# Optimization experiments

Measured on AMD Instinct MI355X. Metric: run time of the kernel, lower is better.

Reference implementation:

```python
import jax, jax.numpy as jnp
import numpy as np

K = 3        # num patches
S = 2        # scale factor
G = 32       # base glimpse size


def _avg_pool(x, k):
    # x: (b, c, H, W), kernel=stride=k (matches F.avg_pool2d(x, k))
    if k == 1:
        return x
    b, c, h, w = x.shape
    return x.reshape(b, c, h // k, k, w // k, k).mean(axis=(3, 5))


def _extract_patch(x, l, size):
    # x: (b, c, h, w); l: (b, 2) in [-1, 1]; returns (b, c, size, size)
    b, c, h, w = x.shape
    start = (0.5 * ((l + 1.0) * h)).astype(jnp.int32)  # (b, 2) [col, row]
    pad = size // 2 + 1
    xp = jnp.pad(x, ((0, 0), (0, 0), (pad, pad), (pad, pad)))

    def slice_one(img, st):
        # img: (c, hp, wp); st: (2,) -> rows use st[1], cols use st[0]
        return jax.lax.dynamic_slice(img, (0, st[1], st[0]), (c, size, size))

    return jax.vmap(slice_one)(xp, start)


def _foveate(x, l):
    phi = []
    size = G
    for _ in range(K):
        phi.append(_extract_patch(x, l, size))
        size = int(S * size)
    # pool every coarser patch back to GxG, concat on channel, flatten
    phi = [_avg_pool(p, p.shape[-1] // G) for p in phi]
    phi = jnp.concatenate(phi, axis=1)          # (b, K*c, G, G)
    return phi.reshape(phi.shape[0], -1)        # (b, K*c*G*G)


def setup_inputs() -> dict:
    key = jax.random.key(0)
    ks = jax.random.split(key, 10)
    b, c, h, w = 256, 3, 224, 224
    h_g = h_l = 1024
    dim = K * G * G * c  # 9216
    x = jax.random.normal(ks[0], (b, c, h, w), dtype=jnp.float32)
    l_prev = jax.random.uniform(ks[1], (b, 2), dtype=jnp.float32, minval=-1.0, maxval=1.0)
    def lin(k, fan_in, fan_out):
        return jax.random.normal(k, (fan_in, fan_out), dtype=jnp.float32) / np.sqrt(fan_in)
    return {
        "x": x, "l_prev": l_prev,
        "W1": lin(ks[2], dim, h_g), "b1": jnp.zeros((h_g,), jnp.float32),
        "W2": lin(ks[3], 2, h_l),   "b2": jnp.zeros((h_l,), jnp.float32),
        "W3": lin(ks[4], h_g, h_g + h_l), "b3": jnp.zeros((h_g + h_l,), jnp.float32),
        "W4": lin(ks[5], h_l, h_g + h_l), "b4": jnp.zeros((h_g + h_l,), jnp.float32),
    }


def reference(x, l_prev, W1, b1, W2, b2, W3, b3, W4, b4):
    glimpse = _foveate(x, l_prev)                       # (b, K*c*G*G)
    g_out = jax.nn.relu(glimpse @ W1 + b1)              # (b, h_g)
    l_out = jax.nn.relu(l_prev @ W2 + b2)               # (b, h_l)
    what = g_out @ W3 + b3                              # (b, h_g+h_l)
    where = l_out @ W4 + b4                             # (b, h_g+h_l)
    return jax.nn.relu(what + where)
```

## Files before the change

### kernel.cpp

```cpp
#include <hip/hip_runtime.h>

typedef __bf16 bf16_t;
typedef __bf16 bf16x8 __attribute__((ext_vector_type(8)));
typedef float f32x4 __attribute__((ext_vector_type(4)));
typedef unsigned short us4 __attribute__((ext_vector_type(4)));
typedef unsigned short us8 __attribute__((ext_vector_type(8)));

template<int F>
__device__ __forceinline__ void fov_scale(const float* __restrict__ xb,
                                          bf16_t* __restrict__ gb,
                                          int r0, int c0, int base, int count, int kidx)
{
  constexpr float inv = 1.0f / (F * F);
  for (int i = threadIdx.x; i < count; i += 256) {
    const int idx = base + i;
    const int ch  = idx >> 10;
    const int rem = idx & 1023;
    const int gy  = rem >> 5, gx = rem & 31;
    const float* xc = xb + ch * 50176;
    float sum = 0.0f;
    const int rbase = r0 + gy * F, cbase = c0 + gx * F;
#pragma unroll
    for (int dy = 0; dy < F; ++dy) {
      const int rr = rbase + dy;
      if ((unsigned)rr < 224u) {
#pragma unroll
        for (int dx = 0; dx < F; ++dx) {
          const int cc = cbase + dx;
          if ((unsigned)cc < 224u) sum += xc[rr * 224 + cc];
        }
      }
    }
    gb[kidx * 3072 + idx] = (bf16_t)(sum * inv);
  }
}

__global__ __launch_bounds__(256) void foveate_kernel(const float* __restrict__ x,
                                                      const float* __restrict__ l,
                                                      bf16_t* __restrict__ g)
{
  const int b = blockIdx.x;
  const float l0 = l[2 * b], l1 = l[2 * b + 1];
  const int st0 = (int)(0.5f * ((l0 + 1.0f) * 224.0f));
  const int st1 = (int)(0.5f * ((l1 + 1.0f) * 224.0f));
  const float* xb = x + (size_t)b * 3 * 50176;
  bf16_t* gb = g + (size_t)b * 9216;
  const int y = blockIdx.y;
  if (y == 0) {
    fov_scale<1>(xb, gb, st1 - 17, st0 - 17, 0, 3072, 0);
  } else if (y <= 2) {
    fov_scale<2>(xb, gb, st1 - 33, st0 - 33, (y - 1) * 1536, 1536, 1);
  } else {
    fov_scale<4>(xb, gb, st1 - 65, st0 - 65, (y - 3) * 768, 768, 2);
  }
}

template<int BM, int BN, int KCHUNK, int NDIM, int KFULL, int KB1>
__global__ __launch_bounds__(256) void gemm_split(const bf16_t* __restrict__ A,
                                                  const float* __restrict__ Bp0,
                                                  const float* __restrict__ Bp1,
                                                  float* __restrict__ part, int Mdim)
{
  constexpr int WROWS = BM / 4;
  constexpr int SM = WROWS / 16;
  constexpr int SN = BN / 16;
  constexpr int LDA = 36;
  __shared__ unsigned short Al[BM * LDA];
  __shared__ unsigned short Bl[BN * LDA];
  const int t = threadIdx.x;
  const int w = t >> 6, lane = t & 63;
  const int lr = lane & 15, kg = lane >> 4;
  const int bm0 = blockIdx.x * BM, bn0 = blockIdx.y * BN;
  const int ks0 = blockIdx.z * KCHUNK;

  f32x4 acc[SM][SN] = {};

  for (int k0 = 0; k0 < KCHUNK; k0 += 32) {
    const int kbase = ks0 + k0;
#pragma unroll
    for (int i = 0; i < BM / 64; ++i) {
      const int q = t + 256 * i;
      const int m = q >> 2, kb = (q & 3) * 8;
      us8 v = *(const us8*)(A + (size_t)(bm0 + m) * KFULL + kbase + kb);
      *(us4*)(&Al[m * LDA + kb])     = __builtin_shufflevector(v, v, 0, 1, 2, 3);
      *(us4*)(&Al[m * LDA + kb + 4]) = __builtin_shufflevector(v, v, 4, 5, 6, 7);
    }
    {
      const int k = t >> 3, nb = (t & 7) * 8;
      const int gk = kbase + k;
      const float* brow = (gk < KB1) ? (Bp0 + (size_t)gk * NDIM)
                                     : (Bp1 + (size_t)(gk - KB1) * NDIM);
      const float4 f0 = *(const float4*)(brow + bn0 + nb);
      const float4 f1 = *(const float4*)(brow + bn0 + nb + 4);
      const float fs[8] = {f0.x, f0.y, f0.z, f0.w, f1.x, f1.y, f1.z, f1.w};
#pragma unroll
      for (int j = 0; j < 8; ++j)
        Bl[(nb + j) * LDA + k] = __builtin_bit_cast(unsigned short, (bf16_t)fs[j]);
    }
    __syncthreads();
    bf16x8 af[SM], bfr[SN];
#pragma unroll
    for (int sm = 0; sm < SM; ++sm) {
      const unsigned short* p = &Al[(w * WROWS + sm * 16 + lr) * LDA + kg * 8];
      us4 x0 = *(const us4*)p;
      us4 x1 = *(const us4*)(p + 4);
      af[sm] = __builtin_bit_cast(bf16x8, __builtin_shufflevector(x0, x1, 0, 1, 2, 3, 4, 5, 6, 7));
    }
#pragma unroll
    for (int sn = 0; sn < SN; ++sn) {
      const unsigned short* p = &Bl[(sn * 16 + lr) * LDA + kg * 8];
      us4 x0 = *(const us4*)p;
      us4 x1 = *(const us4*)(p + 4);
      bfr[sn] = __builtin_bit_cast(bf16x8, __builtin_shufflevector(x0, x1, 0, 1, 2, 3, 4, 5, 6, 7));
    }
#pragma unroll
    for (int sm = 0; sm < SM; ++sm)
#pragma unroll
      for (int sn = 0; sn < SN; ++sn)
        acc[sm][sn] = __builtin_amdgcn_mfma_f32_16x16x32_bf16(af[sm], bfr[sn], acc[sm][sn], 0, 0, 0);
    __syncthreads();
  }
  float* outp = part + (size_t)blockIdx.z * ((size_t)Mdim * NDIM);
#pragma unroll
  for (int sm = 0; sm < SM; ++sm)
#pragma unroll
    for (int sn = 0; sn < SN; ++sn)
#pragma unroll
      for (int r = 0; r < 4; ++r) {
        const int gm = bm0 + w * WROWS + sm * 16 + kg * 4 + r;
        const int gn = bn0 + sn * 16 + lr;
        outp[(size_t)gm * NDIM + gn] = acc[sm][sn][r];
      }
}

__global__ __launch_bounds__(256) void fuse_mid(const float* __restrict__ part1,
                                                const float* __restrict__ b1,
                                                const float* __restrict__ lprev,
                                                const float* __restrict__ W2,
                                                const float* __restrict__ b2,
                                                bf16_t* __restrict__ A2)
{
  const int idx = blockIdx.x * 256 + threadIdx.x;
  const int row = idx >> 11, col = idx & 2047;
  float s;
  if (col < 1024) {
    s = b1[col];
#pragma unroll
    for (int i = 0; i < 8; ++i) s += part1[i * 262144 + row * 1024 + col];
  } else {
    const int n = col - 1024;
    s = fmaf(lprev[2 * row], W2[n], fmaf(lprev[2 * row + 1], W2[1024 + n], b2[n]));
  }
  A2[idx] = (bf16_t)fmaxf(s, 0.0f);
}

__global__ __launch_bounds__(256) void epilogue2(const float* __restrict__ part2,
                                                 const float* __restrict__ b3,
                                                 const float* __restrict__ b4,
                                                 float* __restrict__ out)
{
  const int idx = blockIdx.x * 256 + threadIdx.x;
  const int col = idx & 2047;
  float s = b3[col] + b4[col];
#pragma unroll
  for (int i = 0; i < 4; ++i) s += part2[i * 524288 + idx];
  out[idx] = fmaxf(s, 0.0f);
}

extern "C" void kernel_launch(void* const* d_in, const int* in_sizes, int n_in,
                              void* d_out, int out_size, void* d_ws, size_t ws_size,
                              hipStream_t stream)
{
  const float* x     = (const float*)d_in[0];
  const float* lprev = (const float*)d_in[1];
  const float* W1    = (const float*)d_in[2];
  const float* b1    = (const float*)d_in[3];
  const float* W2    = (const float*)d_in[4];
  const float* b2    = (const float*)d_in[5];
  const float* W3    = (const float*)d_in[6];
  const float* b3    = (const float*)d_in[7];
  const float* W4    = (const float*)d_in[8];
  const float* b4    = (const float*)d_in[9];
  float* out = (float*)d_out;

  char* ws = (char*)d_ws;
  bf16_t* glimpse = (bf16_t*)ws;
  bf16_t* A2      = (bf16_t*)(ws + 4718592);
  float*  part1   = (float*)(ws + 5767168);
  float*  part2   = (float*)(ws + 14155776);

  foveate_kernel<<<dim3(256, 7), 256, 0, stream>>>(x, lprev, glimpse);
  gemm_split<128, 64, 1152, 1024, 9216, 9216>
      <<<dim3(2, 16, 8), 256, 0, stream>>>(glimpse, W1, W1, part1, 256);
  fuse_mid<<<2048, 256, 0, stream>>>(part1, b1, lprev, W2, b2, A2);
  gemm_split<64, 64, 512, 2048, 2048, 1024>
      <<<dim3(4, 32, 4), 256, 0, stream>>>(A2, W3, W4, part2, 256);
  epilogue2<<<2048, 256, 0, stream>>>(part2, b3, b4, out);
}
```

Measured before the change: 319.1 us.

## Pre-transpose weights to bf16, register-prefetch GEMM tiles, deepen split-K

A combined first kernel now runs foveation and also converts W1, W3 and W4 into transposed bf16 copies via shared-memory tile transposes. The GEMMs then read bf16 B tiles with vector loads instead of converting fp32 and doing scattered LDS writes inside the loop. Global loads for the next K step are prefetched into registers while the MFMAs of the current step run. Split-K depth doubles for both GEMMs and BM grows for the second. The cost is an extra full read of all weights plus bf16 writes on every call, and larger partial-sum buffers to reduce.

```diff
diff --git a/kernel.cpp b/kernel.cpp
--- a/kernel.cpp
+++ b/kernel.cpp
@@ -5,6 +5,9 @@
 typedef float f32x4 __attribute__((ext_vector_type(4)));
 typedef unsigned short us4 __attribute__((ext_vector_type(4)));
 typedef unsigned short us8 __attribute__((ext_vector_type(8)));
+
+#define LO4(v) __builtin_shufflevector(v, v, 0, 1, 2, 3)
+#define HI4(v) __builtin_shufflevector(v, v, 4, 5, 6, 7)
 
 template<int F>
 __device__ __forceinline__ void fov_scale(const float* __restrict__ xb,
@@ -35,36 +38,77 @@
   }
 }
 
-__global__ __launch_bounds__(256) void foveate_kernel(const float* __restrict__ x,
-                                                      const float* __restrict__ l,
-                                                      bf16_t* __restrict__ g)
-{
-  const int b = blockIdx.x;
-  const float l0 = l[2 * b], l1 = l[2 * b + 1];
-  const int st0 = (int)(0.5f * ((l0 + 1.0f) * 224.0f));
-  const int st1 = (int)(0.5f * ((l1 + 1.0f) * 224.0f));
-  const float* xb = x + (size_t)b * 3 * 50176;
-  bf16_t* gb = g + (size_t)b * 9216;
-  const int y = blockIdx.y;
-  if (y == 0) {
-    fov_scale<1>(xb, gb, st1 - 17, st0 - 17, 0, 3072, 0);
-  } else if (y <= 2) {
-    fov_scale<2>(xb, gb, st1 - 33, st0 - 33, (y - 1) * 1536, 1536, 1);
+__device__ __forceinline__ void transpose_tile(const float* __restrict__ src, int srcld,
+                                               unsigned short* __restrict__ dst, int dstld)
+{
+  __shared__ unsigned short T[64][72];
+  const int t = threadIdx.x;
+#pragma unroll
+  for (int it = 0; it < 16; ++it) {
+    const int idx = it * 256 + t;
+    const int kk = idx >> 6, nn = idx & 63;
+    T[nn][kk] = __builtin_bit_cast(unsigned short, (bf16_t)src[(size_t)kk * srcld + nn]);
+  }
+  __syncthreads();
+#pragma unroll
+  for (int it = 0; it < 2; ++it) {
+    const int q = it * 256 + t;
+    const int n = q >> 3, kc = (q & 7) * 8;
+    *(us8*)(dst + (size_t)n * dstld + kc) = *(const us8*)&T[n][kc];
+  }
+}
+
+__global__ __launch_bounds__(256) void fov_conv_kernel(const float* __restrict__ x,
+                                                       const float* __restrict__ l,
+                                                       bf16_t* __restrict__ g,
+                                                       const float* __restrict__ W1,
+                                                       const float* __restrict__ W3,
+                                                       const float* __restrict__ W4,
+                                                       bf16_t* __restrict__ W1t,
+                                                       bf16_t* __restrict__ W34t)
+{
+  const int bid = blockIdx.x;
+  if (bid < 1792) {
+    const int b = bid & 255;
+    const int y = bid >> 8;
+    const float l0 = l[2 * b], l1 = l[2 * b + 1];
+    const int st0 = (int)(0.5f * ((l0 + 1.0f) * 224.0f));
+    const int st1 = (int)(0.5f * ((l1 + 1.0f) * 224.0f));
+    const float* xb = x + (size_t)b * 3 * 50176;
+    bf16_t* gb = g + (size_t)b * 9216;
+    if (y == 0) {
+      fov_scale<1>(xb, gb, st1 - 17, st0 - 17, 0, 3072, 0);
+    } else if (y <= 2) {
+      fov_scale<2>(xb, gb, st1 - 33, st0 - 33, (y - 1) * 1536, 1536, 1);
+    } else {
+      fov_scale<4>(xb, gb, st1 - 65, st0 - 65, (y - 3) * 768, 768, 2);
+    }
+  } else if (bid < 4096) {
+    const int cid = bid - 1792;
+    const int kt = cid >> 4, nt = cid & 15;
+    transpose_tile(W1 + (size_t)(kt * 64) * 1024 + nt * 64, 1024,
+                   (unsigned short*)W1t + (size_t)(nt * 64) * 9216 + kt * 64, 9216);
   } else {
-    fov_scale<4>(xb, gb, st1 - 65, st0 - 65, (y - 3) * 768, 768, 2);
-  }
-}
-
-template<int BM, int BN, int KCHUNK, int NDIM, int KFULL, int KB1>
-__global__ __launch_bounds__(256) void gemm_split(const bf16_t* __restrict__ A,
-                                                  const float* __restrict__ Bp0,
-                                                  const float* __restrict__ Bp1,
-                                                  float* __restrict__ part, int Mdim)
+    const int cid = bid - 4096;
+    const int kt = cid >> 5, nt = cid & 31;
+    const int k0 = kt * 64;
+    const float* src = (k0 < 1024) ? (W3 + (size_t)k0 * 2048 + nt * 64)
+                                   : (W4 + (size_t)(k0 - 1024) * 2048 + nt * 64);
+    transpose_tile(src, 2048,
+                   (unsigned short*)W34t + (size_t)(nt * 64) * 2048 + k0, 2048);
+  }
+}
+
+template<int BM, int BN, int KCHUNK, int NDIM, int KFULL>
+__global__ __launch_bounds__(256) void gemm_bb(const bf16_t* __restrict__ A,
+                                               const bf16_t* __restrict__ Bt,
+                                               float* __restrict__ part)
 {
   constexpr int WROWS = BM / 4;
   constexpr int SM = WROWS / 16;
   constexpr int SN = BN / 16;
   constexpr int LDA = 36;
+  constexpr int NLA = BM / 64;
   __shared__ unsigned short Al[BM * LDA];
   __shared__ unsigned short Bl[BN * LDA];
   const int t = threadIdx.x;
@@ -72,32 +116,44 @@
   const int lr = lane & 15, kg = lane >> 4;
   const int bm0 = blockIdx.x * BM, bn0 = blockIdx.y * BN;
   const int ks0 = blockIdx.z * KCHUNK;
+  const unsigned short* Au = (const unsigned short*)A;
+  const unsigned short* Bu = (const unsigned short*)Bt;
+
+  const int bn = t >> 2, bkb = (t & 3) * 8;
+  const bool bld = (t < BN * 4);
 
   f32x4 acc[SM][SN] = {};
+  us8 pa[NLA], pb;
+
+#pragma unroll
+  for (int i = 0; i < NLA; ++i) {
+    const int q = t + 256 * i;
+    pa[i] = *(const us8*)(Au + (size_t)(bm0 + (q >> 2)) * KFULL + ks0 + (q & 3) * 8);
+  }
+  if (bld) pb = *(const us8*)(Bu + (size_t)(bn0 + bn) * KFULL + ks0 + bkb);
 
   for (int k0 = 0; k0 < KCHUNK; k0 += 32) {
-    const int kbase = ks0 + k0;
-#pragma unroll
-    for (int i = 0; i < BM / 64; ++i) {
+#pragma unroll
+    for (int i = 0; i < NLA; ++i) {
       const int q = t + 256 * i;
       const int m = q >> 2, kb = (q & 3) * 8;
-      us8 v = *(const us8*)(A + (size_t)(bm0 + m) * KFULL + kbase + kb);
-      *(us4*)(&Al[m * LDA + kb])     = __builtin_shufflevector(v, v, 0, 1, 2, 3);
-      *(us4*)(&Al[m * LDA + kb + 4]) = __builtin_shufflevector(v, v, 4, 5, 6, 7);
-    }
-    {
-      const int k = t >> 3, nb = (t & 7) * 8;
-      const int gk = kbase + k;
-      const float* brow = (gk < KB1) ? (Bp0 + (size_t)gk * NDIM)
-                                     : (Bp1 + (size_t)(gk - KB1) * NDIM);
-      const float4 f0 = *(const float4*)(brow + bn0 + nb);
-      const float4 f1 = *(const float4*)(brow + bn0 + nb + 4);
-      const float fs[8] = {f0.x, f0.y, f0.z, f0.w, f1.x, f1.y, f1.z, f1.w};
-#pragma unroll
-      for (int j = 0; j < 8; ++j)
-        Bl[(nb + j) * LDA + k] = __builtin_bit_cast(unsigned short, (bf16_t)fs[j]);
+      *(us4*)(&Al[m * LDA + kb])     = LO4(pa[i]);
+      *(us4*)(&Al[m * LDA + kb + 4]) = HI4(pa[i]);
+    }
+    if (bld) {
+      *(us4*)(&Bl[bn * LDA + bkb])     = LO4(pb);
+      *(us4*)(&Bl[bn * LDA + bkb + 4]) = HI4(pb);
     }
     __syncthreads();
+    if (k0 + 32 < KCHUNK) {
+      const int knext = ks0 + k0 + 32;
+#pragma unroll
+      for (int i = 0; i < NLA; ++i) {
+        const int q = t + 256 * i;
+        pa[i] = *(const us8*)(Au + (size_t)(bm0 + (q >> 2)) * KFULL + knext + (q & 3) * 8);
+      }
+      if (bld) pb = *(const us8*)(Bu + (size_t)(bn0 + bn) * KFULL + knext + bkb);
+    }
     bf16x8 af[SM], bfr[SN];
 #pragma unroll
     for (int sm = 0; sm < SM; ++sm) {
@@ -120,7 +176,7 @@
         acc[sm][sn] = __builtin_amdgcn_mfma_f32_16x16x32_bf16(af[sm], bfr[sn], acc[sm][sn], 0, 0, 0);
     __syncthreads();
   }
-  float* outp = part + (size_t)blockIdx.z * ((size_t)Mdim * NDIM);
+  float* outp = part + (size_t)blockIdx.z * ((size_t)256 * NDIM);
 #pragma unroll
   for (int sm = 0; sm < SM; ++sm)
 #pragma unroll
@@ -146,7 +202,7 @@
   if (col < 1024) {
     s = b1[col];
 #pragma unroll
-    for (int i = 0; i < 8; ++i) s += part1[i * 262144 + row * 1024 + col];
+    for (int i = 0; i < 16; ++i) s += part1[i * 262144 + row * 1024 + col];
   } else {
     const int n = col - 1024;
     s = fmaf(lprev[2 * row], W2[n], fmaf(lprev[2 * row + 1], W2[1024 + n], b2[n]));
@@ -163,7 +219,7 @@
   const int col = idx & 2047;
   float s = b3[col] + b4[col];
 #pragma unroll
-  for (int i = 0; i < 4; ++i) s += part2[i * 524288 + idx];
+  for (int i = 0; i < 8; ++i) s += part2[i * 524288 + idx];
   out[idx] = fmaxf(s, 0.0f);
 }
 
@@ -187,13 +243,15 @@
   bf16_t* glimpse = (bf16_t*)ws;
   bf16_t* A2      = (bf16_t*)(ws + 4718592);
   float*  part1   = (float*)(ws + 5767168);
-  float*  part2   = (float*)(ws + 14155776);
-
-  foveate_kernel<<<dim3(256, 7), 256, 0, stream>>>(x, lprev, glimpse);
-  gemm_split<128, 64, 1152, 1024, 9216, 9216>
-      <<<dim3(2, 16, 8), 256, 0, stream>>>(glimpse, W1, W1, part1, 256);
+  float*  part2   = (float*)(ws + 22544384);
+  bf16_t* W1t     = (bf16_t*)(ws + 39321600);
+  bf16_t* W34t    = (bf16_t*)(ws + 58195968);
+
+  fov_conv_kernel<<<5120, 256, 0, stream>>>(x, lprev, glimpse, W1, W3, W4, W1t, W34t);
+  gemm_bb<128, 64, 576, 1024, 9216>
+      <<<dim3(2, 16, 16), 256, 0, stream>>>(glimpse, W1t, part1);
   fuse_mid<<<2048, 256, 0, stream>>>(part1, b1, lprev, W2, b2, A2);
-  gemm_split<64, 64, 512, 2048, 2048, 1024>
-      <<<dim3(4, 32, 4), 256, 0, stream>>>(A2, W3, W4, part2, 256);
+  gemm_bb<128, 64, 256, 2048, 2048>
+      <<<dim3(2, 32, 8), 256, 0, stream>>>(A2, W34t, part2);
   epilogue2<<<2048, 256, 0, stream>>>(part2, b3, b4, out);
 }
```

Result: faster. 287.5 us (-9.9%).
